# Optimization experiments

Hardware: AMD Instinct MI355X
Metric: run time of the kernel (lower is better)

Reference implementation:

```python
import jax, jax.numpy as jnp
import numpy as np

N, L, D, H, R = 16384, 8, 256, 256, 64  # nodes, chain len, input dim, hidden dim, rel dim


def setup_inputs() -> dict:
    key = jax.random.key(0)
    ks = jax.random.split(key, 10)
    s = 1.0 / np.sqrt(H)
    f32 = jnp.float32
    return {
        "left_chain": jax.random.normal(ks[0], (N, L, D), f32),
        "right_chain": jax.random.normal(ks[1], (N, L, D), f32),
        "rel": jax.random.normal(ks[2], (N, R), f32),
        "Wih_l": jax.random.normal(ks[3], (4 * H, D), f32) * s,
        "Whh_l": jax.random.normal(ks[4], (4 * H, H), f32) * s,
        "bih_l": jnp.zeros((4 * H,), f32),
        "bhh_l": jnp.zeros((4 * H,), f32),
        "Wih_r": jax.random.normal(ks[5], (4 * H, D), f32) * s,
        "Whh_r": jax.random.normal(ks[6], (4 * H, H), f32) * s,
        "bih_r": jnp.zeros((4 * H,), f32),
        "bhh_r": jnp.zeros((4 * H,), f32),
        "Wenc": jax.random.normal(ks[7], (H, 2 * H + R), f32) * s,
        "benc": jnp.zeros((H,), f32),
    }


def _lstm_last(x, Wih, Whh, bih, bhh):
    # x: [N, L, D]; PyTorch LSTM gate order i, f, g, o; zero initial state.
    n = x.shape[0]
    h0 = jnp.zeros((n, Whh.shape[1]), x.dtype)
    b = bih + bhh

    def step(carry, xt):
        h, c = carry
        g = xt @ Wih.T + h @ Whh.T + b  # [N, 4H]
        i, f, gg, o = jnp.split(g, 4, axis=-1)
        c = jax.nn.sigmoid(f) * c + jax.nn.sigmoid(i) * jnp.tanh(gg)
        h = jax.nn.sigmoid(o) * jnp.tanh(c)
        return (h, c), None

    (h, _c), _ = jax.lax.scan(step, (h0, h0), jnp.swapaxes(x, 0, 1))
    return h  # final hidden state [N, H]


def reference(left_chain, right_chain, rel,
              Wih_l, Whh_l, bih_l, bhh_l,
              Wih_r, Whh_r, bih_r, bhh_r,
              Wenc, benc):
    hl = _lstm_last(left_chain, Wih_l, Whh_l, bih_l, bhh_l)   # el(t)
    hr = _lstm_last(right_chain, Wih_r, Whh_r, bih_r, bhh_r)  # er(t)
    con = jnp.concatenate([hl, hr, rel], axis=-1)             # [N, 2H+R]
    return jnp.tanh(con @ Wenc.T + benc)                      # enc(t): [N, H]
```

## Files before the change

kernel.cpp:

```cpp
#include <hip/hip_runtime.h>
#include <hip/hip_fp16.h>

#define N_NODES 16384
#define SEQ_L   8
#define DIM_D   256
#define DIM_H   256
#define DIM_R   64

typedef float    f32x4 __attribute__((ext_vector_type(4)));
typedef _Float16 f16x8 __attribute__((ext_vector_type(8)));
typedef _Float16 f16x4 __attribute__((ext_vector_type(4)));

__device__ __forceinline__ float fsig(float x) {
    return __builtin_amdgcn_rcpf(1.f + __expf(-x));
}
__device__ __forceinline__ float ftanh(float x) {
    return 1.f - 2.f * __builtin_amdgcn_rcpf(1.f + __expf(2.f * x));
}

__global__ void cvt6_kernel(const float* __restrict__ s0, const float* __restrict__ s1,
                            const float* __restrict__ s2, const float* __restrict__ s3,
                            const float* __restrict__ s4, const float* __restrict__ s5,
                            _Float16* __restrict__ d0, _Float16* __restrict__ d1,
                            _Float16* __restrict__ d2, _Float16* __restrict__ d3,
                            _Float16* __restrict__ d4, _Float16* __restrict__ d5,
                            int n0, int n1, int n2, int n3, int n4, int n5) {
    const float* S[6] = {s0, s1, s2, s3, s4, s5};
    _Float16*    D[6] = {d0, d1, d2, d3, d4, d5};
    int          Q[6] = {n0 >> 2, n1 >> 2, n2 >> 2, n3 >> 2, n4 >> 2, n5 >> 2};
    const int stride = gridDim.x * blockDim.x;
    const int t0 = blockIdx.x * blockDim.x + threadIdx.x;
    for (int s = 0; s < 6; ++s) {
        const f32x4* src = (const f32x4*)S[s];
        f16x4*       dst = (f16x4*)D[s];
        for (int i = t0; i < Q[s]; i += stride) {
            f32x4 v = src[i];
            f16x4 h;
            h[0] = (_Float16)v[0]; h[1] = (_Float16)v[1];
            h[2] = (_Float16)v[2]; h[3] = (_Float16)v[3];
            dst[i] = h;
        }
    }
}

__global__ __launch_bounds__(512, 2) void lstm_kernel(
    const float* __restrict__ left, const float* __restrict__ right,
    const _Float16* __restrict__ wih_l, const _Float16* __restrict__ whh_l,
    const _Float16* __restrict__ wih_r, const _Float16* __restrict__ whh_r,
    const float* __restrict__ bih_l, const float* __restrict__ bhh_l,
    const float* __restrict__ bih_r, const float* __restrict__ bhh_r,
    _Float16* __restrict__ hl_out, _Float16* __restrict__ hr_out) {

    const int side = blockIdx.y;
    const float*    chain = side ? right : left;
    const _Float16* Wih   = side ? wih_r : wih_l;
    const _Float16* Whh   = side ? whh_r : whh_l;
    const float*    bih   = side ? bih_r : bih_l;
    const float*    bhh   = side ? bhh_r : bhh_l;
    _Float16*       hout  = side ? hr_out : hl_out;

    __shared__ _Float16 lds_x[64 * 256] __attribute__((aligned(16)));
    __shared__ _Float16 lds_h[64 * 256] __attribute__((aligned(16)));

    const int tid  = threadIdx.x;
    const int lane = tid & 63;
    const int wave = tid >> 6;
    const int l15  = lane & 15;
    const int l4   = lane >> 4;
    const int klb  = l4 * 8;
    const int node0 = blockIdx.x * 64;
    const int hid0  = wave * 32;

    const f32x4 FZ = {0.f, 0.f, 0.f, 0.f};

    int   boff[4][2];
    float bias[4][2];
#pragma unroll
    for (int g = 0; g < 4; ++g)
#pragma unroll
        for (int ht = 0; ht < 2; ++ht) {
            int col = g * 256 + hid0 + ht * 16 + l15;
            boff[g][ht] = col * 256 + klb;
            bias[g][ht] = bih[col] + bhh[col];
        }

    f32x4 acc[4][4][2];
    f32x4 cst[4][2];
#pragma unroll
    for (int rt = 0; rt < 4; ++rt)
#pragma unroll
        for (int ht = 0; ht < 2; ++ht) cst[rt][ht] = FZ;

    auto do_gemm = [&](const _Float16* lds, const _Float16* W) {
#pragma unroll
        for (int ks = 0; ks < 8; ++ks) {
            const int kk = ks * 32 + klb;
            f16x8 a[4];
#pragma unroll
            for (int rt = 0; rt < 4; ++rt) {
                int row = rt * 16 + l15;
                int off = row * 256 + (kk ^ ((row & 7) << 3));
                a[rt] = *(const f16x8*)&lds[off];
            }
#pragma unroll
            for (int g = 0; g < 4; ++g)
#pragma unroll
                for (int ht = 0; ht < 2; ++ht) {
                    f16x8 b = *(const f16x8*)&W[boff[g][ht] + ks * 32];
#pragma unroll
                    for (int rt = 0; rt < 4; ++rt)
                        acc[rt][g][ht] = __builtin_amdgcn_mfma_f32_16x16x32_f16(
                            a[rt], b, acc[rt][g][ht], 0, 0, 0);
                }
        }
    };

#pragma unroll 1
    for (int t = 0; t < SEQ_L; ++t) {
#pragma unroll
        for (int it = 0; it < 8; ++it) {
            int e4  = it * 512 + tid;
            int row = e4 >> 6;
            int kq  = (e4 & 63) << 2;
            f32x4 v = *(const f32x4*)(chain +
                      (size_t)(node0 + row) * (SEQ_L * DIM_D) + t * DIM_D + kq);
            f16x4 h4;
            h4[0] = (_Float16)v[0]; h4[1] = (_Float16)v[1];
            h4[2] = (_Float16)v[2]; h4[3] = (_Float16)v[3];
            int idx = row * 256 + (kq ^ ((row & 7) << 3));
            *(f16x4*)&lds_x[idx] = h4;
        }
        __syncthreads();

#pragma unroll
        for (int rt = 0; rt < 4; ++rt)
#pragma unroll
            for (int g = 0; g < 4; ++g)
#pragma unroll
                for (int ht = 0; ht < 2; ++ht) acc[rt][g][ht] = FZ;

        do_gemm(lds_x, Wih);
        if (t > 0) do_gemm(lds_h, Whh);
        __syncthreads();

#pragma unroll
        for (int rt = 0; rt < 4; ++rt)
#pragma unroll
            for (int ht = 0; ht < 2; ++ht)
#pragma unroll
                for (int r = 0; r < 4; ++r) {
                    float gi = acc[rt][0][ht][r] + bias[0][ht];
                    float gf = acc[rt][1][ht][r] + bias[1][ht];
                    float gg = acc[rt][2][ht][r] + bias[2][ht];
                    float go = acc[rt][3][ht][r] + bias[3][ht];
                    float ii = fsig(gi), ff = fsig(gf);
                    float gt = ftanh(gg), oo = fsig(go);
                    float c = ff * cst[rt][ht][r] + ii * gt;
                    cst[rt][ht][r] = c;
                    float h = oo * ftanh(c);
                    int rowl = rt * 16 + l4 * 4 + r;
                    int hid  = hid0 + ht * 16 + l15;
                    lds_h[rowl * 256 + (hid ^ ((rowl & 7) << 3))] = (_Float16)h;
                    if (t == SEQ_L - 1)
                        hout[(size_t)(node0 + rowl) * 256 + hid] = (_Float16)h;
                }
    }
}

__global__ __launch_bounds__(256, 2) void enc_kernel(
    const _Float16* __restrict__ hl, const _Float16* __restrict__ hr,
    const _Float16* __restrict__ rel16, const _Float16* __restrict__ Wenc16,
    const float* __restrict__ benc, float* __restrict__ out) {

    const int tid  = threadIdx.x;
    const int lane = tid & 63;
    const int wave = tid >> 6;
    const int l15  = lane & 15;
    const int l4   = lane >> 4;
    const int klb  = l4 * 8;
    const int row0 = blockIdx.x * 64;
    const int colw = wave * 64;

    const f32x4 FZ = {0.f, 0.f, 0.f, 0.f};
    f32x4 acc[4][4];
#pragma unroll
    for (int rt = 0; rt < 4; ++rt)
#pragma unroll
        for (int ct = 0; ct < 4; ++ct) acc[rt][ct] = FZ;

    float bce[4];
#pragma unroll
    for (int ct = 0; ct < 4; ++ct) bce[ct] = benc[colw + ct * 16 + l15];

    for (int ks = 0; ks < 18; ++ks) {
        const int kk = ks * 32 + klb;
        f16x8 a[4];
#pragma unroll
        for (int rt = 0; rt < 4; ++rt) {
            int row = row0 + rt * 16 + l15;
            const _Float16* p;
            if (ks < 8)       p = hl    + (size_t)row * 256 + kk;
            else if (ks < 16) p = hr    + (size_t)row * 256 + (kk - 256);
            else              p = rel16 + (size_t)row * 64  + (kk - 512);
            a[rt] = *(const f16x8*)p;
        }
#pragma unroll
        for (int ct = 0; ct < 4; ++ct) {
            int col = colw + ct * 16 + l15;
            f16x8 b = *(const f16x8*)&Wenc16[(size_t)col * 576 + kk];
#pragma unroll
            for (int rt = 0; rt < 4; ++rt)
                acc[rt][ct] = __builtin_amdgcn_mfma_f32_16x16x32_f16(
                    a[rt], b, acc[rt][ct], 0, 0, 0);
        }
    }

#pragma unroll
    for (int rt = 0; rt < 4; ++rt)
#pragma unroll
        for (int ct = 0; ct < 4; ++ct)
#pragma unroll
            for (int r = 0; r < 4; ++r) {
                int row = row0 + rt * 16 + l4 * 4 + r;
                int col = colw + ct * 16 + l15;
                out[(size_t)row * 256 + col] = ftanh(acc[rt][ct][r] + bce[ct]);
            }
}

extern "C" void kernel_launch(void* const* d_in, const int* in_sizes, int n_in,
                              void* d_out, int out_size, void* d_ws, size_t ws_size,
                              hipStream_t stream) {
    const float* left  = (const float*)d_in[0];
    const float* right = (const float*)d_in[1];
    const float* rel   = (const float*)d_in[2];
    const float* Wih_l = (const float*)d_in[3];
    const float* Whh_l = (const float*)d_in[4];
    const float* bih_l = (const float*)d_in[5];
    const float* bhh_l = (const float*)d_in[6];
    const float* Wih_r = (const float*)d_in[7];
    const float* Whh_r = (const float*)d_in[8];
    const float* bih_r = (const float*)d_in[9];
    const float* bhh_r = (const float*)d_in[10];
    const float* Wenc  = (const float*)d_in[11];
    const float* benc  = (const float*)d_in[12];
    float* out = (float*)d_out;

    char* ws = (char*)d_ws;
    _Float16* wih_l16 = (_Float16*)(ws);
    _Float16* whh_l16 = (_Float16*)(ws + 512 * 1024);
    _Float16* wih_r16 = (_Float16*)(ws + 1024 * 1024);
    _Float16* whh_r16 = (_Float16*)(ws + 1536 * 1024);
    _Float16* wenc16  = (_Float16*)(ws + 2048 * 1024);
    _Float16* rel16   = (_Float16*)(ws + 2560 * 1024);
    _Float16* hl16    = (_Float16*)(ws + 4608 * 1024);
    _Float16* hr16    = (_Float16*)(ws + 4608 * 1024 + 8192 * 1024);
    (void)in_sizes; (void)n_in; (void)out_size; (void)ws_size;

    hipLaunchKernelGGL(cvt6_kernel, dim3(512), dim3(256), 0, stream,
                       Wih_l, Whh_l, Wih_r, Whh_r, Wenc, rel,
                       wih_l16, whh_l16, wih_r16, whh_r16, wenc16, rel16,
                       4 * DIM_H * DIM_D, 4 * DIM_H * DIM_H,
                       4 * DIM_H * DIM_D, 4 * DIM_H * DIM_H,
                       DIM_H * (2 * DIM_H + DIM_R), N_NODES * DIM_R);

    hipLaunchKernelGGL(lstm_kernel, dim3(N_NODES / 64, 2), dim3(512), 0, stream,
                       left, right, wih_l16, whh_l16, wih_r16, whh_r16,
                       bih_l, bhh_l, bih_r, bhh_r, hl16, hr16);

    hipLaunchKernelGGL(enc_kernel, dim3(N_NODES / 64), dim3(256), 0, stream,
                       hl16, hr16, rel16, wenc16, benc, out);
}
```

Measured before the change: 1.502 ms.

## Pre-pack weights into MFMA fragment order and coalesce LSTM output stores

The prep kernel now converts the LSTM and encoder weights to fp16 in an MFMA-fragment-contiguous layout. Each wave's B-operand load becomes one contiguous 1 KB read instead of a strided gather over 16 weight rows. The input chain loads are marked nontemporal. The final hidden state is written once after the loop from LDS with coalesced 16-byte nontemporal stores, replacing scattered 2-byte stores. The pack kernel uses integer division per element, which adds a little prep cost.

```diff
diff --git a/kernel.cpp b/kernel.cpp
--- a/kernel.cpp
+++ b/kernel.cpp
@@ -18,43 +18,67 @@
     return 1.f - 2.f * __builtin_amdgcn_rcpf(1.f + __expf(2.f * x));
 }
 
-__global__ void cvt6_kernel(const float* __restrict__ s0, const float* __restrict__ s1,
-                            const float* __restrict__ s2, const float* __restrict__ s3,
-                            const float* __restrict__ s4, const float* __restrict__ s5,
-                            _Float16* __restrict__ d0, _Float16* __restrict__ d1,
-                            _Float16* __restrict__ d2, _Float16* __restrict__ d3,
-                            _Float16* __restrict__ d4, _Float16* __restrict__ d5,
-                            int n0, int n1, int n2, int n3, int n4, int n5) {
-    const float* S[6] = {s0, s1, s2, s3, s4, s5};
-    _Float16*    D[6] = {d0, d1, d2, d3, d4, d5};
-    int          Q[6] = {n0 >> 2, n1 >> 2, n2 >> 2, n3 >> 2, n4 >> 2, n5 >> 2};
+__device__ __forceinline__ void pack_w(const float* __restrict__ W, _Float16* __restrict__ P,
+                                       int n_colgrp, int n_ks, int Kdim,
+                                       int t0, int stride) {
+    const int total = n_colgrp * n_ks * 64;
+    for (int i = t0; i < total; i += stride) {
+        int colgrp = i / (n_ks * 64);
+        int rem    = i - colgrp * (n_ks * 64);
+        int ks     = rem >> 6;
+        int lane   = rem & 63;
+        int srow   = colgrp * 16 + (lane & 15);
+        int sk     = ks * 32 + (lane >> 4) * 8;
+        const float* s = W + (size_t)srow * Kdim + sk;
+        f32x4 v0 = *(const f32x4*)s;
+        f32x4 v1 = *(const f32x4*)(s + 4);
+        f16x8 h;
+        h[0] = (_Float16)v0[0]; h[1] = (_Float16)v0[1];
+        h[2] = (_Float16)v0[2]; h[3] = (_Float16)v0[3];
+        h[4] = (_Float16)v1[0]; h[5] = (_Float16)v1[1];
+        h[6] = (_Float16)v1[2]; h[7] = (_Float16)v1[3];
+        *(f16x8*)&P[(size_t)i * 8] = h;
+    }
+}
+
+__global__ void prep_kernel(const float* __restrict__ Wih_l, const float* __restrict__ Whh_l,
+                            const float* __restrict__ Wih_r, const float* __restrict__ Whh_r,
+                            const float* __restrict__ Wenc,  const float* __restrict__ rel,
+                            _Float16* __restrict__ pih_l, _Float16* __restrict__ phh_l,
+                            _Float16* __restrict__ pih_r, _Float16* __restrict__ phh_r,
+                            _Float16* __restrict__ penc,  _Float16* __restrict__ rel16) {
     const int stride = gridDim.x * blockDim.x;
     const int t0 = blockIdx.x * blockDim.x + threadIdx.x;
-    for (int s = 0; s < 6; ++s) {
-        const f32x4* src = (const f32x4*)S[s];
-        f16x4*       dst = (f16x4*)D[s];
-        for (int i = t0; i < Q[s]; i += stride) {
-            f32x4 v = src[i];
-            f16x4 h;
-            h[0] = (_Float16)v[0]; h[1] = (_Float16)v[1];
-            h[2] = (_Float16)v[2]; h[3] = (_Float16)v[3];
-            dst[i] = h;
-        }
+    pack_w(Wih_l, pih_l, 64, 8, 256, t0, stride);
+    pack_w(Whh_l, phh_l, 64, 8, 256, t0, stride);
+    pack_w(Wih_r, pih_r, 64, 8, 256, t0, stride);
+    pack_w(Whh_r, phh_r, 64, 8, 256, t0, stride);
+    pack_w(Wenc,  penc,  16, 18, 576, t0, stride);
+    const int nq = (N_NODES * DIM_R) / 8;
+    for (int i = t0; i < nq; i += stride) {
+        f32x4 v0 = *(const f32x4*)(rel + (size_t)i * 8);
+        f32x4 v1 = *(const f32x4*)(rel + (size_t)i * 8 + 4);
+        f16x8 h;
+        h[0] = (_Float16)v0[0]; h[1] = (_Float16)v0[1];
+        h[2] = (_Float16)v0[2]; h[3] = (_Float16)v0[3];
+        h[4] = (_Float16)v1[0]; h[5] = (_Float16)v1[1];
+        h[6] = (_Float16)v1[2]; h[7] = (_Float16)v1[3];
+        *(f16x8*)&rel16[(size_t)i * 8] = h;
     }
 }
 
 __global__ __launch_bounds__(512, 2) void lstm_kernel(
     const float* __restrict__ left, const float* __restrict__ right,
-    const _Float16* __restrict__ wih_l, const _Float16* __restrict__ whh_l,
-    const _Float16* __restrict__ wih_r, const _Float16* __restrict__ whh_r,
+    const _Float16* __restrict__ pih_l, const _Float16* __restrict__ phh_l,
+    const _Float16* __restrict__ pih_r, const _Float16* __restrict__ phh_r,
     const float* __restrict__ bih_l, const float* __restrict__ bhh_l,
     const float* __restrict__ bih_r, const float* __restrict__ bhh_r,
     _Float16* __restrict__ hl_out, _Float16* __restrict__ hr_out) {
 
     const int side = blockIdx.y;
     const float*    chain = side ? right : left;
-    const _Float16* Wih   = side ? wih_r : wih_l;
-    const _Float16* Whh   = side ? whh_r : whh_l;
+    const _Float16* Pih   = side ? pih_r : pih_l;
+    const _Float16* Phh   = side ? phh_r : phh_l;
     const float*    bih   = side ? bih_r : bih_l;
     const float*    bhh   = side ? bhh_r : bhh_l;
     _Float16*       hout  = side ? hr_out : hl_out;
@@ -73,16 +97,16 @@
 
     const f32x4 FZ = {0.f, 0.f, 0.f, 0.f};
 
-    int   boff[4][2];
     float bias[4][2];
 #pragma unroll
     for (int g = 0; g < 4; ++g)
 #pragma unroll
         for (int ht = 0; ht < 2; ++ht) {
             int col = g * 256 + hid0 + ht * 16 + l15;
-            boff[g][ht] = col * 256 + klb;
             bias[g][ht] = bih[col] + bhh[col];
         }
+
+    const int cg0 = wave * 2;
 
     f32x4 acc[4][4][2];
     f32x4 cst[4][2];
@@ -91,7 +115,7 @@
 #pragma unroll
         for (int ht = 0; ht < 2; ++ht) cst[rt][ht] = FZ;
 
-    auto do_gemm = [&](const _Float16* lds, const _Float16* W) {
+    auto do_gemm = [&](const _Float16* lds, const _Float16* P) {
 #pragma unroll
         for (int ks = 0; ks < 8; ++ks) {
             const int kk = ks * 32 + klb;
@@ -106,7 +130,7 @@
             for (int g = 0; g < 4; ++g)
 #pragma unroll
                 for (int ht = 0; ht < 2; ++ht) {
-                    f16x8 b = *(const f16x8*)&W[boff[g][ht] + ks * 32];
+                    f16x8 b = *(const f16x8*)&P[(((g * 16 + cg0 + ht) * 8 + ks) << 9) + (lane << 3)];
 #pragma unroll
                     for (int rt = 0; rt < 4; ++rt)
                         acc[rt][g][ht] = __builtin_amdgcn_mfma_f32_16x16x32_f16(
@@ -122,8 +146,8 @@
             int e4  = it * 512 + tid;
             int row = e4 >> 6;
             int kq  = (e4 & 63) << 2;
-            f32x4 v = *(const f32x4*)(chain +
-                      (size_t)(node0 + row) * (SEQ_L * DIM_D) + t * DIM_D + kq);
+            f32x4 v = __builtin_nontemporal_load((const f32x4*)(chain +
+                      (size_t)(node0 + row) * (SEQ_L * DIM_D) + t * DIM_D + kq));
             f16x4 h4;
             h4[0] = (_Float16)v[0]; h4[1] = (_Float16)v[1];
             h4[2] = (_Float16)v[2]; h4[3] = (_Float16)v[3];
@@ -139,8 +163,8 @@
 #pragma unroll
                 for (int ht = 0; ht < 2; ++ht) acc[rt][g][ht] = FZ;
 
-        do_gemm(lds_x, Wih);
-        if (t > 0) do_gemm(lds_h, Whh);
+        do_gemm(lds_x, Pih);
+        if (t > 0) do_gemm(lds_h, Phh);
         __syncthreads();
 
 #pragma unroll
@@ -161,15 +185,26 @@
                     int rowl = rt * 16 + l4 * 4 + r;
                     int hid  = hid0 + ht * 16 + l15;
                     lds_h[rowl * 256 + (hid ^ ((rowl & 7) << 3))] = (_Float16)h;
-                    if (t == SEQ_L - 1)
-                        hout[(size_t)(node0 + rowl) * 256 + hid] = (_Float16)h;
                 }
+    }
+
+    __syncthreads();
+    {
+        int row = tid >> 3;
+        int seg = (tid & 7) * 32;
+        _Float16* dst = hout + (size_t)(node0 + row) * 256 + seg;
+        int sw = (row & 7) << 3;
+#pragma unroll
+        for (int j = 0; j < 4; ++j) {
+            f16x8 v = *(const f16x8*)&lds_h[row * 256 + ((seg + j * 8) ^ sw)];
+            __builtin_nontemporal_store(v, (f16x8*)(dst + j * 8));
+        }
     }
 }
 
 __global__ __launch_bounds__(256, 2) void enc_kernel(
     const _Float16* __restrict__ hl, const _Float16* __restrict__ hr,
-    const _Float16* __restrict__ rel16, const _Float16* __restrict__ Wenc16,
+    const _Float16* __restrict__ rel16, const _Float16* __restrict__ penc,
     const float* __restrict__ benc, float* __restrict__ out) {
 
     const int tid  = threadIdx.x;
@@ -206,8 +241,7 @@
         }
 #pragma unroll
         for (int ct = 0; ct < 4; ++ct) {
-            int col = colw + ct * 16 + l15;
-            f16x8 b = *(const f16x8*)&Wenc16[(size_t)col * 576 + kk];
+            f16x8 b = *(const f16x8*)&penc[((((wave * 4 + ct) * 18 + ks)) << 9) + (lane << 3)];
 #pragma unroll
             for (int rt = 0; rt < 4; ++rt)
                 acc[rt][ct] = __builtin_amdgcn_mfma_f32_16x16x32_f16(
@@ -246,27 +280,24 @@
     float* out = (float*)d_out;
 
     char* ws = (char*)d_ws;
-    _Float16* wih_l16 = (_Float16*)(ws);
-    _Float16* whh_l16 = (_Float16*)(ws + 512 * 1024);
-    _Float16* wih_r16 = (_Float16*)(ws + 1024 * 1024);
-    _Float16* whh_r16 = (_Float16*)(ws + 1536 * 1024);
-    _Float16* wenc16  = (_Float16*)(ws + 2048 * 1024);
-    _Float16* rel16   = (_Float16*)(ws + 2560 * 1024);
-    _Float16* hl16    = (_Float16*)(ws + 4608 * 1024);
-    _Float16* hr16    = (_Float16*)(ws + 4608 * 1024 + 8192 * 1024);
+    _Float16* pih_l = (_Float16*)(ws);
+    _Float16* phh_l = (_Float16*)(ws + 512 * 1024);
+    _Float16* pih_r = (_Float16*)(ws + 1024 * 1024);
+    _Float16* phh_r = (_Float16*)(ws + 1536 * 1024);
+    _Float16* penc  = (_Float16*)(ws + 2048 * 1024);
+    _Float16* rel16 = (_Float16*)(ws + 2560 * 1024);
+    _Float16* hl16  = (_Float16*)(ws + 4608 * 1024);
+    _Float16* hr16  = (_Float16*)(ws + 4608 * 1024 + 8192 * 1024);
     (void)in_sizes; (void)n_in; (void)out_size; (void)ws_size;
 
-    hipLaunchKernelGGL(cvt6_kernel, dim3(512), dim3(256), 0, stream,
+    hipLaunchKernelGGL(prep_kernel, dim3(512), dim3(256), 0, stream,
                        Wih_l, Whh_l, Wih_r, Whh_r, Wenc, rel,
-                       wih_l16, whh_l16, wih_r16, whh_r16, wenc16, rel16,
-                       4 * DIM_H * DIM_D, 4 * DIM_H * DIM_H,
-                       4 * DIM_H * DIM_D, 4 * DIM_H * DIM_H,
-                       DIM_H * (2 * DIM_H + DIM_R), N_NODES * DIM_R);
+                       pih_l, phh_l, pih_r, phh_r, penc, rel16);
 
     hipLaunchKernelGGL(lstm_kernel, dim3(N_NODES / 64, 2), dim3(512), 0, stream,
-                       left, right, wih_l16, whh_l16, wih_r16, whh_r16,
+                       left, right, pih_l, phh_l, pih_r, phh_r,
                        bih_l, bhh_l, bih_r, bhh_r, hl16, hr16);
 
     hipLaunchKernelGGL(enc_kernel, dim3(N_NODES / 64), dim3(256), 0, stream,
-                       hl16, hr16, rel16, wenc16, benc, out);
-}
+                       hl16, hr16, rel16, penc, benc, out);
+}
```

New measurement: 1.534 ms. +2.2%, slower.
